# Kernel tuning notes

Measured on AMD Instinct MI355X. Metric: run time of the kernel, lower is better.

## Reference

```python
import jax, jax.numpy as jnp
from jax import lax
from jax.scipy.special import logsumexp
import numpy as np

N_NODES = 6144
N_EDGES = 98304
N_FEAT = 128
N_TPLT = 16
M_NODES = 10
N_CG = 5        # conditional-gradient (Frank-Wolfe) outer iterations
N_SINK = 50     # log-domain Sinkhorn iterations for the linearized OT subproblem


def setup_inputs() -> dict:
    key = jax.random.key(0)
    k1, k2, k3, k4 = jax.random.split(key, 4)
    x = jax.random.normal(k1, (N_NODES, N_FEAT), dtype=jnp.float32)
    edge_index = jax.random.randint(k2, (2, N_EDGES), 0, N_NODES, dtype=jnp.int64)
    # template_initialisation: uniform(0,1) adjacencies, symmetrized; normal features; zero q0/alpha0
    t_raw = jax.random.uniform(k3, (N_TPLT, M_NODES, M_NODES), dtype=jnp.float32)
    templates = 0.5 * (t_raw + jnp.transpose(t_raw, (0, 2, 1)))
    templates_features = jax.random.normal(k4, (N_TPLT, M_NODES, N_FEAT), dtype=jnp.float32)
    q0 = jnp.zeros((N_TPLT, M_NODES), dtype=jnp.float32)
    alpha0 = jnp.zeros((1,), dtype=jnp.float32)
    return {"x": x, "edge_index": edge_index, "templates": templates,
            "templates_features": templates_features, "q0": q0, "alpha0": alpha0}


def _sinkhorn_log(G, logp, logq, reg):
    """Log-domain Sinkhorn solving min <G,T> + reg*H(T) over U(p,q)."""
    K = -G / reg                         # [n, m]
    f0 = jnp.zeros_like(logp)

    def body(f, _):
        g = logq - logsumexp(K + f[:, None], axis=0)
        f = logp - logsumexp(K + g[None, :], axis=1)
        return f, None

    f, _ = lax.scan(body, f0, None, length=N_SINK)
    g = logq - logsumexp(K + f[:, None], axis=0)
    return jnp.exp(f[:, None] + K + g[None, :])


def _fgw2(M, C1, C2, p, q, alpha):
    """Fused Gromov-Wasserstein distance (square loss) via conditional gradient.
    M: [n,m] feature cost, C1: [n,n] graph structure, C2: [m,m] template structure."""
    # init_matrix (square loss): constC = f1(C1) p 1^T + 1 q^T f2(C2)^T
    constC = (C1 ** 2 @ p)[:, None] + (C2 ** 2 @ q)[None, :]   # [n, m]
    logp, logq = jnp.log(p), jnp.log(q)
    T0 = p[:, None] * q[None, :]

    def step(T, _):
        C1TC2 = C1 @ T @ C2                                   # [n, m] (dominant cost)
        grad = (1.0 - alpha) * M + alpha * 2.0 * (constC - 2.0 * C1TC2)
        reg = lax.stop_gradient(0.05 * jnp.max(jnp.abs(grad)) + 1e-8)
        Tn = _sinkhorn_log(grad, logp, logq, reg)             # linearized OT subproblem
        dT = Tn - T
        # exact line search for the quadratic objective along dT
        C1dTC2 = C1 @ dT @ C2
        a = -2.0 * alpha * jnp.sum(C1dTC2 * dT)
        b = (1.0 - alpha) * jnp.sum(M * dT) + alpha * (jnp.sum(constC * dT) - 4.0 * jnp.sum(C1TC2 * dT))
        tau = jnp.where(a > 0.0,
                        jnp.clip(-b / (2.0 * a + 1e-16), 0.0, 1.0),
                        jnp.where(a + b < 0.0, 1.0, 0.0))
        return T + tau * dT, None

    T, _ = lax.scan(step, T0, None, length=N_CG)
    gw = jnp.sum((constC - 2.0 * (C1 @ T @ C2)) * T)
    wass = jnp.sum(M * T)
    return (1.0 - alpha) * wass + alpha * gw


def reference(x, edge_index, templates, templates_features, q0, alpha0):
    alpha = jax.nn.sigmoid(alpha0)[0]
    q = jax.nn.softmax(q0, axis=1)                            # [T, m] template node weights
    n = x.shape[0]
    # dense adjacency from edge list (symmetrized)
    A = jnp.zeros((n, n), dtype=x.dtype).at[edge_index[0], edge_index[1]].set(1.0)
    C1 = jnp.maximum(A, A.T)                                  # [n, n]
    p = jnp.full((n,), 1.0 / n, dtype=x.dtype)
    # squared euclidean feature cost per template: [T, n, m]
    M = (jnp.sum(x ** 2, axis=1)[None, :, None]
         + jnp.sum(templates_features ** 2, axis=-1)[:, None, :]
         - 2.0 * jnp.einsum('nf,tmf->tnm', x, templates_features))
    dists = jax.vmap(_fgw2, in_axes=(0, None, 0, None, 0, None))(M, C1, templates, p, q, alpha)
    return dists                                              # [n_templates]
```

## Files before the change

### kernel.cpp

```cpp
#include <hip/hip_runtime.h>
#include <hip/hip_cooperative_groups.h>

namespace cgx = cooperative_groups;

static constexpr int NN  = 6144;
static constexpr int NE  = 98304;
static constexpr int NF  = 128;
static constexpr int NT  = 16;
static constexpr int MN  = 10;
static constexpr int NCG = 5;
static constexpr int NSK = 50;
static constexpr int WPR = NN / 32;
static constexpr int TPB = 768;
static constexpr int NBLK = 256;
static constexpr int RPT = NN / TPB;
static constexpr int NW  = TPB / 64;

static_assert(TPB * RPT == NN, "row mapping");

static constexpr size_t OFF_M   = 0;
static constexpr size_t OFF_T4  = OFF_M  + (size_t)NT * NN * MN;
static constexpr size_t OFF_T1  = OFF_T4 + (size_t)NT * NN * 4;
static constexpr size_t OFF_C4  = OFF_T1 + (size_t)NT * NN;
static constexpr size_t OFF_C1  = OFF_C4 + (size_t)NT * NN * 4;
static constexpr size_t OFF_D4  = OFF_C1 + (size_t)NT * NN;
static constexpr size_t OFF_D1  = OFF_D4 + (size_t)NT * NN * 4;
static constexpr size_t OFF_RS  = OFF_D1 + (size_t)NT * NN;
static constexpr size_t OFF_DEG = OFF_RS + NN;
static constexpr size_t OFF_CI  = OFF_DEG + NN;
static constexpr size_t OFF_NNZ = OFF_CI + NE;

static constexpr int LDS_PL  = NN * 20;
static constexpr int LDS_SP  = TPB * 7 * 4;
static constexpr int LDS_DYN = LDS_PL + LDS_SP;

__device__ __forceinline__ unsigned f2bf(float f) {
    unsigned u = __float_as_uint(f);
    return (u + 0x7fffu + ((u >> 16) & 1u)) >> 16;
}
__device__ __forceinline__ unsigned packbf(float a, float b) { return f2bf(a) | (f2bf(b) << 16); }
__device__ __forceinline__ float bflo(unsigned w) { return __uint_as_float(w << 16); }
__device__ __forceinline__ float bfhi(unsigned w) { return __uint_as_float(w & 0xffff0000u); }

extern __shared__ char sMem[];

__global__ __launch_bounds__(TPB) void tfgw_kernel(
    const float* __restrict__ x, const void* __restrict__ eiv,
    const float* __restrict__ tpl, const float* __restrict__ tf,
    const float* __restrict__ q0, const float* __restrict__ a0,
    float* __restrict__ out, float* __restrict__ W)
{
    __shared__ float sC2[MN * MN];
    __shared__ float sq[MN], scq[MN], sqC2[MN], sNSQ[MN];
    __shared__ unsigned svp[5];
    __shared__ unsigned svP2[5];
    __shared__ float sCv[5];
    __shared__ float sRed[3 * NW];
    __shared__ float sBC[2];
    __shared__ float sDots[4];

    const int tid = threadIdx.x;
    const int bid = blockIdx.x;

    unsigned* BM    = (unsigned*)(W + OFF_T4);
    int* rowst      = (int*)(W + OFF_RS);
    int* degi       = (int*)(W + OFF_DEG);
    unsigned short* colix = (unsigned short*)(W + OFF_CI);
    int* nnzc       = (int*)(W + OFF_NNZ);
    float* Mw  = W + OFF_M;

    uint4*    PL4x = (uint4*)sMem;
    unsigned* PL1x = (unsigned*)(sMem + NN * 16);
    unsigned* sPp  = (unsigned*)(sMem + LDS_PL);

    const float alpha  = 1.f / (1.f + __expf(-a0[0]));
    const float invn   = 1.f / (float)NN;
    const float alpha2 = 2.f * alpha;
    const float oma    = 1.f - alpha;

    cgx::grid_group grid = cgx::this_grid();

    for (int idx = bid * TPB + tid; idx < NN * WPR; idx += NBLK * TPB) BM[idx] = 0u;
    if (bid == 0 && tid == 0) *nnzc = 0;
    grid.sync();

    {
        const unsigned* uw = (const unsigned*)eiv;
        const bool is64 = (uw[1] == 0u && uw[3] == 0u && uw[5] == 0u);
        for (int e = bid * TPB + tid; e < NE; e += NBLK * TPB) {
            int s, d;
            if (is64) {
                s = (int)((const long long*)eiv)[e];
                d = (int)((const long long*)eiv)[NE + e];
            } else {
                s = ((const int*)eiv)[e];
                d = ((const int*)eiv)[NE + e];
            }
            atomicOr(&BM[(size_t)s * WPR + (d >> 5)], 1u << (d & 31));
            atomicOr(&BM[(size_t)d * WPR + (s >> 5)], 1u << (s & 31));
        }
        float* sTF = (float*)sMem;
        const int t = bid >> 4, rb = bid & 15;
        for (int k = tid; k < MN * NF; k += TPB) sTF[k] = tf[t * MN * NF + k];
        __syncthreads();
        if (tid < MN) {
            float s = 0.f;
            for (int k = 0; k < NF; ++k) { float v = sTF[tid * NF + k]; s += v * v; }
            sNSQ[tid] = s;
        }
        __syncthreads();
        if (tid < 384) {
            const int i = rb * 384 + tid;
            const float4* x4 = (const float4*)(x + (size_t)i * NF);
            const float4* t4 = (const float4*)sTF;
            float acc[MN]; float xn = 0.f;
            #pragma unroll
            for (int j = 0; j < MN; ++j) acc[j] = 0.f;
            for (int k4 = 0; k4 < NF / 4; ++k4) {
                float4 xv = x4[k4];
                xn += xv.x * xv.x + xv.y * xv.y + xv.z * xv.z + xv.w * xv.w;
                #pragma unroll
                for (int j = 0; j < MN; ++j) {
                    float4 tv = t4[j * (NF / 4) + k4];
                    acc[j] += xv.x * tv.x + xv.y * tv.y + xv.z * tv.z + xv.w * tv.w;
                }
            }
            float* Mrow = Mw + (size_t)t * NN * MN + (size_t)i * MN;
            #pragma unroll
            for (int j = 0; j < MN; ++j) Mrow[j] = xn + sNSQ[j] - 2.f * acc[j];
        }
    }
    grid.sync();

    {
        const int i = bid * TPB + tid;
        if (i < NN) {
            int cnt = 0;
            for (int w = 0; w < WPR; ++w) cnt += __popc(BM[(size_t)i * WPR + w]);
            int st = atomicAdd(nnzc, cnt);
            rowst[i] = st; degi[i] = cnt;
            int p = st;
            for (int w = 0; w < WPR; ++w) {
                unsigned m = BM[(size_t)i * WPR + w];
                while (m) { int b = __ffs(m) - 1; m &= m - 1; colix[p++] = (unsigned short)((w << 5) + b); }
            }
        }
    }
    grid.sync();

    if (bid >= NT) return;

    const int t = bid;
    float* Mb = Mw + (size_t)t * NN * MN;
    uint4*    Tb4 = (uint4*)(W + OFF_T4) + (size_t)t * NN;
    unsigned* Tb1 = (unsigned*)(W + OFF_T1) + (size_t)t * NN;
    uint4*    Cb4 = (uint4*)(W + OFF_C4) + (size_t)t * NN;
    unsigned* Cb1 = (unsigned*)(W + OFF_C1) + (size_t)t * NN;
    uint4*    Db4 = (uint4*)(W + OFF_D4) + (size_t)t * NN;
    unsigned* Db1 = (unsigned*)(W + OFF_D1) + (size_t)t * NN;

    if (tid == 0) {
        float qv[MN]; float qm = -1e30f;
        for (int j = 0; j < MN; ++j) { qv[j] = q0[t * MN + j]; qm = fmaxf(qm, qv[j]); }
        float qs = 0.f;
        for (int j = 0; j < MN; ++j) { qv[j] = __expf(qv[j] - qm); qs += qv[j]; }
        for (int j = 0; j < MN; ++j) { qv[j] /= qs; sq[j] = qv[j]; }
        for (int j = 0; j < MN; ++j) {
            float s2 = 0.f, s1 = 0.f;
            for (int k = 0; k < MN; ++k) {
                float cjk = tpl[t * MN * MN + j * MN + k];
                s2 += cjk * cjk * qv[k];
                s1 += tpl[t * MN * MN + k * MN + j] * qv[k];
            }
            scq[j] = s2; sqC2[j] = s1;
        }
    }
    for (int k = tid; k < MN * MN; k += TPB) sC2[k] = tpl[t * MN * MN + k];
    __syncthreads();

    for (int cgi = 0; cgi < NCG; ++cgi) {
        if (tid == 0) {
            float tau = 0.f;
            if (cgi > 0) {
                float a = -2.f * alpha * sDots[3];
                float b = oma * sDots[0] + alpha * (sDots[1] - 4.f * sDots[2]);
                if (a > 0.f) tau = fminf(fmaxf(-b / (2.f * a + 1e-16f), 0.f), 1.f);
                else         tau = (a + b < 0.f) ? 1.f : 0.f;
            }
            sBC[0] = tau;
        }
        if (tid < 5) svP2[tid] = 0xFFFFFFFFu;
        __syncthreads();
        const float tau = sBC[0];
        if (cgi > 0 && tau == 0.f) break;

        float gmax = 0.f;
        #pragma unroll
        for (int k = 0; k < RPT; ++k) {
            const int r = tid + k * TPB;
            const float cp = (float)degi[r] * invn;
            float C[MN];
            if (cgi == 0) {
                uint4 tw4; unsigned tw1;
                uint4 cw4; unsigned cw1;
                tw4.x = packbf(sq[0]*invn, sq[1]*invn); tw4.y = packbf(sq[2]*invn, sq[3]*invn);
                tw4.z = packbf(sq[4]*invn, sq[5]*invn); tw4.w = packbf(sq[6]*invn, sq[7]*invn);
                tw1   = packbf(sq[8]*invn, sq[9]*invn);
                cw4.x = packbf(cp*sqC2[0], cp*sqC2[1]); cw4.y = packbf(cp*sqC2[2], cp*sqC2[3]);
                cw4.z = packbf(cp*sqC2[4], cp*sqC2[5]); cw4.w = packbf(cp*sqC2[6], cp*sqC2[7]);
                cw1   = packbf(cp*sqC2[8], cp*sqC2[9]);
                Tb4[r] = tw4; Tb1[r] = tw1; Cb4[r] = cw4; Cb1[r] = cw1;
                C[0]=bflo(cw4.x); C[1]=bfhi(cw4.x); C[2]=bflo(cw4.y); C[3]=bfhi(cw4.y);
                C[4]=bflo(cw4.z); C[5]=bfhi(cw4.z); C[6]=bflo(cw4.w); C[7]=bfhi(cw4.w);
                C[8]=bflo(cw1);   C[9]=bfhi(cw1);
            } else {
                float dd[MN];
                uint4 a = PL4x[r]; unsigned b4 = PL1x[r];
                dd[0]=bflo(a.x); dd[1]=bfhi(a.x); dd[2]=bflo(a.y); dd[3]=bfhi(a.y);
                dd[4]=bflo(a.z); dd[5]=bfhi(a.z); dd[6]=bflo(a.w); dd[7]=bfhi(a.w);
                dd[8]=bflo(b4);  dd[9]=bfhi(b4);
                uint4 tw4 = Tb4[r]; unsigned tw1 = Tb1[r];
                uint4 cw4 = Cb4[r]; unsigned cw1 = Cb1[r];
                uint4 Dw4 = Db4[r]; unsigned Dw1 = Db1[r];
                float T[MN], Dd[MN];
                T[0]=bflo(tw4.x); T[1]=bfhi(tw4.x); T[2]=bflo(tw4.y); T[3]=bfhi(tw4.y);
                T[4]=bflo(tw4.z); T[5]=bfhi(tw4.z); T[6]=bflo(tw4.w); T[7]=bfhi(tw4.w);
                T[8]=bflo(tw1);   T[9]=bfhi(tw1);
                C[0]=bflo(cw4.x); C[1]=bfhi(cw4.x); C[2]=bflo(cw4.y); C[3]=bfhi(cw4.y);
                C[4]=bflo(cw4.z); C[5]=bfhi(cw4.z); C[6]=bflo(cw4.w); C[7]=bfhi(cw4.w);
                C[8]=bflo(cw1);   C[9]=bfhi(cw1);
                Dd[0]=bflo(Dw4.x); Dd[1]=bfhi(Dw4.x); Dd[2]=bflo(Dw4.y); Dd[3]=bfhi(Dw4.y);
                Dd[4]=bflo(Dw4.z); Dd[5]=bfhi(Dw4.z); Dd[6]=bflo(Dw4.w); Dd[7]=bfhi(Dw4.w);
                Dd[8]=bflo(Dw1);   Dd[9]=bfhi(Dw1);
                #pragma unroll
                for (int j = 0; j < MN; ++j) { T[j] += tau * dd[j]; C[j] += tau * Dd[j]; }
                uint4 ntw4; unsigned ntw1; uint4 ncw4; unsigned ncw1;
                ntw4.x = packbf(T[0],T[1]); ntw4.y = packbf(T[2],T[3]);
                ntw4.z = packbf(T[4],T[5]); ntw4.w = packbf(T[6],T[7]);
                ntw1   = packbf(T[8],T[9]);
                ncw4.x = packbf(C[0],C[1]); ncw4.y = packbf(C[2],C[3]);
                ncw4.z = packbf(C[4],C[5]); ncw4.w = packbf(C[6],C[7]);
                ncw1   = packbf(C[8],C[9]);
                Tb4[r] = ntw4; Tb1[r] = ntw1; Cb4[r] = ncw4; Cb1[r] = ncw1;
                C[0]=bflo(ncw4.x); C[1]=bfhi(ncw4.x); C[2]=bflo(ncw4.y); C[3]=bfhi(ncw4.y);
                C[4]=bflo(ncw4.z); C[5]=bfhi(ncw4.z); C[6]=bflo(ncw4.w); C[7]=bfhi(ncw4.w);
                C[8]=bflo(ncw1);   C[9]=bfhi(ncw1);
            }
            float g[MN];
            #pragma unroll
            for (int h = 0; h < 5; ++h) {
                float2 mv = *(const float2*)(Mb + (size_t)r * MN + 2*h);
                g[2*h]   = oma * mv.x + alpha2 * (cp + scq[2*h]   - 2.f * C[2*h]);
                g[2*h+1] = oma * mv.y + alpha2 * (cp + scq[2*h+1] - 2.f * C[2*h+1]);
                gmax = fmaxf(gmax, fmaxf(__builtin_fabsf(g[2*h]), __builtin_fabsf(g[2*h+1])));
            }
            PL4x[r] = make_uint4(packbf(g[0],g[1]), packbf(g[2],g[3]),
                                 packbf(g[4],g[5]), packbf(g[6],g[7]));
            PL1x[r] = packbf(g[8], g[9]);
        }
        #pragma unroll
        for (int d = 32; d; d >>= 1) gmax = fmaxf(gmax, __shfl_xor(gmax, d));
        if ((tid & 63) == 0) sRed[tid >> 6] = gmax;
        __syncthreads();
        if (tid == 0) {
            float m = sRed[0];
            for (int w = 1; w < NW; ++w) m = fmaxf(m, sRed[w]);
            sBC[1] = 1.f / (0.05f * m + 1e-8f);
        }
        __syncthreads();
        const float invreg = sBC[1];

        #pragma unroll
        for (int k = 0; k < RPT; ++k) {
            const int r = tid + k * TPB;
            uint4 a = PL4x[r]; unsigned b4 = PL1x[r];
            float g[MN];
            g[0]=bflo(a.x); g[1]=bfhi(a.x); g[2]=bflo(a.y); g[3]=bfhi(a.y);
            g[4]=bflo(a.z); g[5]=bfhi(a.z); g[6]=bflo(a.w); g[7]=bfhi(a.w);
            g[8]=bflo(b4);  g[9]=bfhi(b4);
            float e[MN];
            #pragma unroll
            for (int j = 0; j < MN; ++j) e[j] = __expf(-g[j] * invreg);
            PL4x[r] = make_uint4(packbf(e[0],e[1]), packbf(e[2],e[3]),
                                 packbf(e[4],e[5]), packbf(e[6],e[7]));
            PL1x[r] = packbf(e[8], e[9]);
        }

        if (cgi == 0) {
            float a[MN];
            #pragma unroll
            for (int j = 0; j < MN; ++j) a[j] = 0.f;
            #pragma unroll
            for (int k = 0; k < RPT; ++k) {
                const int r = tid + k * TPB;
                uint4 q = PL4x[r]; unsigned b4 = PL1x[r];
                a[0]+=bflo(q.x); a[1]+=bfhi(q.x); a[2]+=bflo(q.y); a[3]+=bfhi(q.y);
                a[4]+=bflo(q.z); a[5]+=bfhi(q.z); a[6]+=bflo(q.w); a[7]+=bfhi(q.w);
                a[8]+=bflo(b4);  a[9]+=bfhi(b4);
            }
            #pragma unroll
            for (int p = 0; p < 5; ++p) sPp[tid * 7 + p] = packbf(a[2*p], a[2*p+1]);
            __syncthreads();
            if (tid < 320) {
                const int p = tid >> 6, c = tid & 63;
                float s0 = 0.f, s1 = 0.f;
                #pragma unroll
                for (int kk = 0; kk < NW; ++kk) {
                    unsigned w = sPp[(c + (kk << 6)) * 7 + p];
                    s0 += bflo(w); s1 += bfhi(w);
                }
                #pragma unroll
                for (int d = 32; d; d >>= 1) { s0 += __shfl_xor(s0, d); s1 += __shfl_xor(s1, d); }
                if (c == 0) svp[p] = packbf(sq[2*p] / s0, sq[2*p+1] / s1);
            }
            __syncthreads();
        }

        for (int it = 1; it <= NSK; ++it) {
            float vv[MN];
            #pragma unroll
            for (int p = 0; p < 5; ++p) {
                unsigned w = svp[p];
                vv[2*p] = bflo(w); vv[2*p+1] = bfhi(w);
            }
            float a[MN];
            #pragma unroll
            for (int j = 0; j < MN; ++j) a[j] = 0.f;
            #pragma unroll
            for (int k = 0; k < RPT; ++k) {
                const int r = tid + k * TPB;
                uint4 q = PL4x[r]; unsigned b4 = PL1x[r];
                float e[MN];
                e[0]=bflo(q.x); e[1]=bfhi(q.x); e[2]=bflo(q.y); e[3]=bfhi(q.y);
                e[4]=bflo(q.z); e[5]=bfhi(q.z); e[6]=bflo(q.w); e[7]=bfhi(q.w);
                e[8]=bflo(b4);  e[9]=bfhi(b4);
                float R = 0.f;
                #pragma unroll
                for (int j = 0; j < MN; ++j) R += e[j] * vv[j];
                const float u = invn * __builtin_amdgcn_rcpf(R);
                #pragma unroll
                for (int j = 0; j < MN; ++j) a[j] += e[j] * u;
            }
            #pragma unroll
            for (int p = 0; p < 5; ++p) sPp[tid * 7 + p] = packbf(a[2*p], a[2*p+1]);
            __syncthreads();
            if (tid < 320) {
                const int p = tid >> 6, c = tid & 63;
                float s0 = 0.f, s1 = 0.f;
                #pragma unroll
                for (int kk = 0; kk < NW; ++kk) {
                    unsigned w = sPp[(c + (kk << 6)) * 7 + p];
                    s0 += bflo(w); s1 += bfhi(w);
                }
                #pragma unroll
                for (int d = 32; d; d >>= 1) { s0 += __shfl_xor(s0, d); s1 += __shfl_xor(s1, d); }
                if (c == 0) {
                    unsigned pw = packbf(sq[2*p] / s0, sq[2*p+1] / s1);
                    unsigned old = svp[p], old2 = svP2[p];
                    sCv[p] = (pw == old || pw == old2) ? 1.f : 0.f;
                    svP2[p] = old;
                    svp[p] = pw;
                }
            }
            __syncthreads();
            if (sCv[0] + sCv[1] + sCv[2] + sCv[3] + sCv[4] == 5.f) break;
        }

        {
            float vv[MN];
            #pragma unroll
            for (int p = 0; p < 5; ++p) {
                unsigned w = svp[p];
                vv[2*p] = bflo(w); vv[2*p+1] = bfhi(w);
            }
            float sMdT = 0.f, sCdT = 0.f, sCTdT = 0.f;
            #pragma unroll
            for (int k = 0; k < RPT; ++k) {
                const int r = tid + k * TPB;
                const float cp = (float)degi[r] * invn;
                uint4 q = PL4x[r]; unsigned b4 = PL1x[r];
                float e[MN], dd[MN];
                e[0]=bflo(q.x); e[1]=bfhi(q.x); e[2]=bflo(q.y); e[3]=bfhi(q.y);
                e[4]=bflo(q.z); e[5]=bfhi(q.z); e[6]=bflo(q.w); e[7]=bfhi(q.w);
                e[8]=bflo(b4);  e[9]=bfhi(b4);
                float R = 0.f;
                #pragma unroll
                for (int j = 0; j < MN; ++j) R += e[j] * vv[j];
                const float u = invn * __builtin_amdgcn_rcpf(R);
                uint4 tw4 = Tb4[r]; unsigned tw1 = Tb1[r];
                uint4 cw4 = Cb4[r]; unsigned cw1 = Cb1[r];
                float T[MN], C[MN];
                T[0]=bflo(tw4.x); T[1]=bfhi(tw4.x); T[2]=bflo(tw4.y); T[3]=bfhi(tw4.y);
                T[4]=bflo(tw4.z); T[5]=bfhi(tw4.z); T[6]=bflo(tw4.w); T[7]=bfhi(tw4.w);
                T[8]=bflo(tw1);   T[9]=bfhi(tw1);
                C[0]=bflo(cw4.x); C[1]=bfhi(cw4.x); C[2]=bflo(cw4.y); C[3]=bfhi(cw4.y);
                C[4]=bflo(cw4.z); C[5]=bfhi(cw4.z); C[6]=bflo(cw4.w); C[7]=bfhi(cw4.w);
                C[8]=bflo(cw1);   C[9]=bfhi(cw1);
                #pragma unroll
                for (int h = 0; h < 5; ++h) {
                    float2 mv = *(const float2*)(Mb + (size_t)r * MN + 2*h);
                    float d0 = u * e[2*h]   * vv[2*h]   - T[2*h];
                    float d1 = u * e[2*h+1] * vv[2*h+1] - T[2*h+1];
                    dd[2*h] = d0; dd[2*h+1] = d1;
                    sMdT  += mv.x * d0 + mv.y * d1;
                    sCdT  += (cp + scq[2*h]) * d0 + (cp + scq[2*h+1]) * d1;
                    sCTdT += C[2*h] * d0 + C[2*h+1] * d1;
                }
                PL4x[r] = make_uint4(packbf(dd[0],dd[1]), packbf(dd[2],dd[3]),
                                     packbf(dd[4],dd[5]), packbf(dd[6],dd[7]));
                PL1x[r] = packbf(dd[8], dd[9]);
            }
            #pragma unroll
            for (int d = 32; d; d >>= 1) {
                sMdT  += __shfl_xor(sMdT, d);
                sCdT  += __shfl_xor(sCdT, d);
                sCTdT += __shfl_xor(sCTdT, d);
            }
            if ((tid & 63) == 0) {
                const int w = tid >> 6;
                sRed[w] = sMdT; sRed[NW + w] = sCdT; sRed[2*NW + w] = sCTdT;
            }
            __syncthreads();
            if (tid == 0) {
                float r0 = 0.f, r1 = 0.f, r2 = 0.f;
                for (int w = 0; w < NW; ++w) { r0 += sRed[w]; r1 += sRed[NW+w]; r2 += sRed[2*NW+w]; }
                sDots[0] = r0; sDots[1] = r1; sDots[2] = r2;
            }
        }

        {
            float dot = 0.f;
            #pragma unroll
            for (int k = 0; k < RPT; ++k) {
                const int r = tid + k * TPB;
                float y[MN];
                #pragma unroll
                for (int j = 0; j < MN; ++j) y[j] = 0.f;
                const int st = rowst[r], dg = degi[r];
                const unsigned short* cl = colix + st;
                for (int e = 0; e < dg; ++e) {
                    const int j = cl[e];
                    uint4 q = PL4x[j]; unsigned b4 = PL1x[j];
                    y[0] += bflo(q.x); y[1] += bfhi(q.x);
                    y[2] += bflo(q.y); y[3] += bfhi(q.y);
                    y[4] += bflo(q.z); y[5] += bfhi(q.z);
                    y[6] += bflo(q.w); y[7] += bfhi(q.w);
                    y[8] += bflo(b4);  y[9] += bfhi(b4);
                }
                uint4 q = PL4x[r]; unsigned b4 = PL1x[r];
                float dd[MN];
                dd[0]=bflo(q.x); dd[1]=bfhi(q.x); dd[2]=bflo(q.y); dd[3]=bfhi(q.y);
                dd[4]=bflo(q.z); dd[5]=bfhi(q.z); dd[6]=bflo(q.w); dd[7]=bfhi(q.w);
                dd[8]=bflo(b4);  dd[9]=bfhi(b4);
                float o[MN];
                #pragma unroll
                for (int h = 0; h < 5; ++h) {
                    float o0 = 0.f, o1 = 0.f;
                    #pragma unroll
                    for (int j = 0; j < MN; ++j) {
                        o0 += y[j] * sC2[j * MN + 2*h];
                        o1 += y[j] * sC2[j * MN + 2*h + 1];
                    }
                    o[2*h] = o0; o[2*h+1] = o1;
                    dot += o0 * dd[2*h] + o1 * dd[2*h+1];
                }
                Db4[r] = make_uint4(packbf(o[0],o[1]), packbf(o[2],o[3]),
                                    packbf(o[4],o[5]), packbf(o[6],o[7]));
                Db1[r] = packbf(o[8], o[9]);
            }
            #pragma unroll
            for (int d = 32; d; d >>= 1) dot += __shfl_xor(dot, d);
            if ((tid & 63) == 0) sRed[tid >> 6] = dot;
            __syncthreads();
            if (tid == 0) {
                float s = 0.f;
                for (int w = 0; w < NW; ++w) s += sRed[w];
                sDots[3] = s;
            }
            __syncthreads();
        }
    }

    if (tid == 0) {
        float a = -2.f * alpha * sDots[3];
        float b = oma * sDots[0] + alpha * (sDots[1] - 4.f * sDots[2]);
        float tau;
        if (a > 0.f) tau = fminf(fmaxf(-b / (2.f * a + 1e-16f), 0.f), 1.f);
        else         tau = (a + b < 0.f) ? 1.f : 0.f;
        sBC[0] = tau;
    }
    __syncthreads();
    {
        const float tau = sBC[0];
        float gw = 0.f, wass = 0.f;
        #pragma unroll
        for (int k = 0; k < RPT; ++k) {
            const int r = tid + k * TPB;
            const float cp = (float)degi[r] * invn;
            uint4 q = PL4x[r]; unsigned b4 = PL1x[r];
            float dd[MN];
            dd[0]=bflo(q.x); dd[1]=bfhi(q.x); dd[2]=bflo(q.y); dd[3]=bfhi(q.y);
            dd[4]=bflo(q.z); dd[5]=bfhi(q.z); dd[6]=bflo(q.w); dd[7]=bfhi(q.w);
            dd[8]=bflo(b4);  dd[9]=bfhi(b4);
            uint4 tw4 = Tb4[r]; unsigned tw1 = Tb1[r];
            uint4 cw4 = Cb4[r]; unsigned cw1 = Cb1[r];
            uint4 Dw4 = Db4[r]; unsigned Dw1 = Db1[r];
            float T[MN], C[MN], Dd[MN];
            T[0]=bflo(tw4.x); T[1]=bfhi(tw4.x); T[2]=bflo(tw4.y); T[3]=bfhi(tw4.y);
            T[4]=bflo(tw4.z); T[5]=bfhi(tw4.z); T[6]=bflo(tw4.w); T[7]=bfhi(tw4.w);
            T[8]=bflo(tw1);   T[9]=bfhi(tw1);
            C[0]=bflo(cw4.x); C[1]=bfhi(cw4.x); C[2]=bflo(cw4.y); C[3]=bfhi(cw4.y);
            C[4]=bflo(cw4.z); C[5]=bfhi(cw4.z); C[6]=bflo(cw4.w); C[7]=bfhi(cw4.w);
            C[8]=bflo(cw1);   C[9]=bfhi(cw1);
            Dd[0]=bflo(Dw4.x); Dd[1]=bfhi(Dw4.x); Dd[2]=bflo(Dw4.y); Dd[3]=bfhi(Dw4.y);
            Dd[4]=bflo(Dw4.z); Dd[5]=bfhi(Dw4.z); Dd[6]=bflo(Dw4.w); Dd[7]=bfhi(Dw4.w);
            Dd[8]=bflo(Dw1);   Dd[9]=bfhi(Dw1);
            #pragma unroll
            for (int h = 0; h < 5; ++h) {
                float2 mv = *(const float2*)(Mb + (size_t)r * MN + 2*h);
                float Tf0 = T[2*h]   + tau * dd[2*h];
                float Tf1 = T[2*h+1] + tau * dd[2*h+1];
                float Cf0 = C[2*h]   + tau * Dd[2*h];
                float Cf1 = C[2*h+1] + tau * Dd[2*h+1];
                gw   += (cp + scq[2*h]   - 2.f * Cf0) * Tf0
                      + (cp + scq[2*h+1] - 2.f * Cf1) * Tf1;
                wass += mv.x * Tf0 + mv.y * Tf1;
            }
        }
        #pragma unroll
        for (int d = 32; d; d >>= 1) {
            gw   += __shfl_xor(gw, d);
            wass += __shfl_xor(wass, d);
        }
        if ((tid & 63) == 0) { sRed[tid >> 6] = gw; sRed[NW + (tid >> 6)] = wass; }
        __syncthreads();
        if (tid == 0) {
            float g = 0.f, ws = 0.f;
            for (int w = 0; w < NW; ++w) { g += sRed[w]; ws += sRed[NW + w]; }
            out[t] = oma * ws + alpha * g;
        }
    }
}

extern "C" void kernel_launch(void* const* d_in, const int* in_sizes, int n_in,
                              void* d_out, int out_size, void* d_ws, size_t ws_size,
                              hipStream_t stream) {
    const float* x   = (const float*)d_in[0];
    const void*  ei  = d_in[1];
    const float* tpl = (const float*)d_in[2];
    const float* tfp = (const float*)d_in[3];
    const float* q0  = (const float*)d_in[4];
    const float* a0  = (const float*)d_in[5];
    float* outp = (float*)d_out;
    float* Wp   = (float*)d_ws;
    (void)hipFuncSetAttribute(reinterpret_cast<const void*>(&tfgw_kernel),
                              hipFuncAttributeMaxDynamicSharedMemorySize, LDS_DYN);
    void* args[] = { &x, &ei, &tpl, &tfp, &q0, &a0, &outp, &Wp };
    hipLaunchCooperativeKernel(reinterpret_cast<const void*>(&tfgw_kernel),
                               dim3(NBLK), dim3(TPB), args, LDS_DYN, stream);
}
```

Measured before the change: 713.1 us.

## Keep Sinkhorn kernel values in registers and drop convergence early-exit

The exponentiated kernel values per row (packed bf16) now live in a per-thread register array instead of LDS, which removes repeated LDS reads in every Sinkhorn iteration. A waves-per-EU attribute is added so the compiler can budget the extra registers. The two-step fixed-point convergence check and its early break are removed, so every Sinkhorn iteration now runs in full. This saves a sync and some bookkeeping per iteration but loses the early exit.

```diff
diff --git a/kernel.cpp b/kernel.cpp
--- a/kernel.cpp
+++ b/kernel.cpp
@@ -44,7 +44,8 @@
 
 extern __shared__ char sMem[];
 
-__global__ __launch_bounds__(TPB) void tfgw_kernel(
+__global__ __launch_bounds__(TPB) __attribute__((amdgpu_waves_per_eu(3, 3)))
+void tfgw_kernel(
     const float* __restrict__ x, const void* __restrict__ eiv,
     const float* __restrict__ tpl, const float* __restrict__ tf,
     const float* __restrict__ q0, const float* __restrict__ a0,
@@ -53,8 +54,6 @@
     __shared__ float sC2[MN * MN];
     __shared__ float sq[MN], scq[MN], sqC2[MN], sNSQ[MN];
     __shared__ unsigned svp[5];
-    __shared__ unsigned svP2[5];
-    __shared__ float sCv[5];
     __shared__ float sRed[3 * NW];
     __shared__ float sBC[2];
     __shared__ float sDots[4];
@@ -178,6 +177,8 @@
     for (int k = tid; k < MN * MN; k += TPB) sC2[k] = tpl[t * MN * MN + k];
     __syncthreads();
 
+    unsigned Ep[RPT * 5];
+
     for (int cgi = 0; cgi < NCG; ++cgi) {
         if (tid == 0) {
             float tau = 0.f;
@@ -189,7 +190,6 @@
             }
             sBC[0] = tau;
         }
-        if (tid < 5) svP2[tid] = 0xFFFFFFFFu;
         __syncthreads();
         const float tau = sBC[0];
         if (cgi > 0 && tau == 0.f) break;
@@ -201,8 +201,7 @@
             const float cp = (float)degi[r] * invn;
             float C[MN];
             if (cgi == 0) {
-                uint4 tw4; unsigned tw1;
-                uint4 cw4; unsigned cw1;
+                uint4 tw4; unsigned tw1; uint4 cw4; unsigned cw1;
                 tw4.x = packbf(sq[0]*invn, sq[1]*invn); tw4.y = packbf(sq[2]*invn, sq[3]*invn);
                 tw4.z = packbf(sq[4]*invn, sq[5]*invn); tw4.w = packbf(sq[6]*invn, sq[7]*invn);
                 tw1   = packbf(sq[8]*invn, sq[9]*invn);
@@ -234,17 +233,16 @@
                 Dd[8]=bflo(Dw1);   Dd[9]=bfhi(Dw1);
                 #pragma unroll
                 for (int j = 0; j < MN; ++j) { T[j] += tau * dd[j]; C[j] += tau * Dd[j]; }
-                uint4 ntw4; unsigned ntw1; uint4 ncw4; unsigned ncw1;
-                ntw4.x = packbf(T[0],T[1]); ntw4.y = packbf(T[2],T[3]);
-                ntw4.z = packbf(T[4],T[5]); ntw4.w = packbf(T[6],T[7]);
-                ntw1   = packbf(T[8],T[9]);
-                ncw4.x = packbf(C[0],C[1]); ncw4.y = packbf(C[2],C[3]);
-                ncw4.z = packbf(C[4],C[5]); ncw4.w = packbf(C[6],C[7]);
-                ncw1   = packbf(C[8],C[9]);
-                Tb4[r] = ntw4; Tb1[r] = ntw1; Cb4[r] = ncw4; Cb1[r] = ncw1;
-                C[0]=bflo(ncw4.x); C[1]=bfhi(ncw4.x); C[2]=bflo(ncw4.y); C[3]=bfhi(ncw4.y);
-                C[4]=bflo(ncw4.z); C[5]=bfhi(ncw4.z); C[6]=bflo(ncw4.w); C[7]=bfhi(ncw4.w);
-                C[8]=bflo(ncw1);   C[9]=bfhi(ncw1);
+                uint4 n4; unsigned n1;
+                n4.x = packbf(T[0],T[1]); n4.y = packbf(T[2],T[3]);
+                n4.z = packbf(T[4],T[5]); n4.w = packbf(T[6],T[7]); n1 = packbf(T[8],T[9]);
+                Tb4[r] = n4; Tb1[r] = n1;
+                n4.x = packbf(C[0],C[1]); n4.y = packbf(C[2],C[3]);
+                n4.z = packbf(C[4],C[5]); n4.w = packbf(C[6],C[7]); n1 = packbf(C[8],C[9]);
+                Cb4[r] = n4; Cb1[r] = n1;
+                C[0]=bflo(n4.x); C[1]=bfhi(n4.x); C[2]=bflo(n4.y); C[3]=bfhi(n4.y);
+                C[4]=bflo(n4.z); C[5]=bfhi(n4.z); C[6]=bflo(n4.w); C[7]=bfhi(n4.w);
+                C[8]=bflo(n1);   C[9]=bfhi(n1);
             }
             float g[MN];
             #pragma unroll
@@ -254,9 +252,8 @@
                 g[2*h+1] = oma * mv.y + alpha2 * (cp + scq[2*h+1] - 2.f * C[2*h+1]);
                 gmax = fmaxf(gmax, fmaxf(__builtin_fabsf(g[2*h]), __builtin_fabsf(g[2*h+1])));
             }
-            PL4x[r] = make_uint4(packbf(g[0],g[1]), packbf(g[2],g[3]),
-                                 packbf(g[4],g[5]), packbf(g[6],g[7]));
-            PL1x[r] = packbf(g[8], g[9]);
+            #pragma unroll
+            for (int h = 0; h < 5; ++h) Ep[k*5 + h] = packbf(g[2*h], g[2*h+1]);
         }
         #pragma unroll
         for (int d = 32; d; d >>= 1) gmax = fmaxf(gmax, __shfl_xor(gmax, d));
@@ -271,33 +268,24 @@
         const float invreg = sBC[1];
 
         #pragma unroll
-        for (int k = 0; k < RPT; ++k) {
-            const int r = tid + k * TPB;
-            uint4 a = PL4x[r]; unsigned b4 = PL1x[r];
-            float g[MN];
-            g[0]=bflo(a.x); g[1]=bfhi(a.x); g[2]=bflo(a.y); g[3]=bfhi(a.y);
-            g[4]=bflo(a.z); g[5]=bfhi(a.z); g[6]=bflo(a.w); g[7]=bfhi(a.w);
-            g[8]=bflo(b4);  g[9]=bfhi(b4);
-            float e[MN];
-            #pragma unroll
-            for (int j = 0; j < MN; ++j) e[j] = __expf(-g[j] * invreg);
-            PL4x[r] = make_uint4(packbf(e[0],e[1]), packbf(e[2],e[3]),
-                                 packbf(e[4],e[5]), packbf(e[6],e[7]));
-            PL1x[r] = packbf(e[8], e[9]);
-        }
+        for (int k = 0; k < RPT; ++k)
+            #pragma unroll
+            for (int h = 0; h < 5; ++h) {
+                unsigned w = Ep[k*5 + h];
+                Ep[k*5 + h] = packbf(__expf(-bflo(w) * invreg), __expf(-bfhi(w) * invreg));
+            }
 
         if (cgi == 0) {
             float a[MN];
             #pragma unroll
             for (int j = 0; j < MN; ++j) a[j] = 0.f;
             #pragma unroll
-            for (int k = 0; k < RPT; ++k) {
-                const int r = tid + k * TPB;
-                uint4 q = PL4x[r]; unsigned b4 = PL1x[r];
-                a[0]+=bflo(q.x); a[1]+=bfhi(q.x); a[2]+=bflo(q.y); a[3]+=bfhi(q.y);
-                a[4]+=bflo(q.z); a[5]+=bfhi(q.z); a[6]+=bflo(q.w); a[7]+=bfhi(q.w);
-                a[8]+=bflo(b4);  a[9]+=bfhi(b4);
-            }
+            for (int k = 0; k < RPT; ++k)
+                #pragma unroll
+                for (int h = 0; h < 5; ++h) {
+                    unsigned w = Ep[k*5 + h];
+                    a[2*h] += bflo(w); a[2*h+1] += bfhi(w);
+                }
             #pragma unroll
             for (int p = 0; p < 5; ++p) sPp[tid * 7 + p] = packbf(a[2*p], a[2*p+1]);
             __syncthreads();
@@ -328,12 +316,12 @@
             for (int j = 0; j < MN; ++j) a[j] = 0.f;
             #pragma unroll
             for (int k = 0; k < RPT; ++k) {
-                const int r = tid + k * TPB;
-                uint4 q = PL4x[r]; unsigned b4 = PL1x[r];
                 float e[MN];
-                e[0]=bflo(q.x); e[1]=bfhi(q.x); e[2]=bflo(q.y); e[3]=bfhi(q.y);
-                e[4]=bflo(q.z); e[5]=bfhi(q.z); e[6]=bflo(q.w); e[7]=bfhi(q.w);
-                e[8]=bflo(b4);  e[9]=bfhi(b4);
+                #pragma unroll
+                for (int h = 0; h < 5; ++h) {
+                    unsigned w = Ep[k*5 + h];
+                    e[2*h] = bflo(w); e[2*h+1] = bfhi(w);
+                }
                 float R = 0.f;
                 #pragma unroll
                 for (int j = 0; j < MN; ++j) R += e[j] * vv[j];
@@ -354,16 +342,9 @@
                 }
                 #pragma unroll
                 for (int d = 32; d; d >>= 1) { s0 += __shfl_xor(s0, d); s1 += __shfl_xor(s1, d); }
-                if (c == 0) {
-                    unsigned pw = packbf(sq[2*p] / s0, sq[2*p+1] / s1);
-                    unsigned old = svp[p], old2 = svP2[p];
-                    sCv[p] = (pw == old || pw == old2) ? 1.f : 0.f;
-                    svP2[p] = old;
-                    svp[p] = pw;
-                }
-            }
-            __syncthreads();
-            if (sCv[0] + sCv[1] + sCv[2] + sCv[3] + sCv[4] == 5.f) break;
+                if (c == 0) svp[p] = packbf(sq[2*p] / s0, sq[2*p+1] / s1);
+            }
+            __syncthreads();
         }
 
         {
@@ -378,11 +359,12 @@
             for (int k = 0; k < RPT; ++k) {
                 const int r = tid + k * TPB;
                 const float cp = (float)degi[r] * invn;
-                uint4 q = PL4x[r]; unsigned b4 = PL1x[r];
                 float e[MN], dd[MN];
-                e[0]=bflo(q.x); e[1]=bfhi(q.x); e[2]=bflo(q.y); e[3]=bfhi(q.y);
-                e[4]=bflo(q.z); e[5]=bfhi(q.z); e[6]=bflo(q.w); e[7]=bfhi(q.w);
-                e[8]=bflo(b4);  e[9]=bfhi(b4);
+                #pragma unroll
+                for (int h = 0; h < 5; ++h) {
+                    unsigned w = Ep[k*5 + h];
+                    e[2*h] = bflo(w); e[2*h+1] = bfhi(w);
+                }
                 float R = 0.f;
                 #pragma unroll
                 for (int j = 0; j < MN; ++j) R += e[j] * vv[j];
```

Result: slower. 1.022 ms (+43.3%).
